# Kernel optimization log

Hardware: AMD Instinct MI355X
Metric: run time of the kernel (lower is better)

Reference implementation:

```python
import jax, jax.numpy as jnp
import numpy as np
import math

EPS = 1e-8      # module eps for log/clamp
BN_EPS = 1e-5   # torch BatchNorm1d default eps


def _bn(h, g, b, m, v):
    # eval-mode BatchNorm1d over channel dim of (B, C, P)
    scale = g / jnp.sqrt(v + BN_EPS)
    return (h - m[None, :, None]) * scale[None, :, None] + b[None, :, None]


def _conv(h, W, b):
    # Conv1d with kernel_size=1 == per-point channel mixing
    return jnp.einsum('oc,bcp->bop', W, h) + b[None, :, None]


def _pairwise_lv_fts(xi, xj, eps=EPS):
    # ParT pairwise Lorentz-vector features, num_outputs=4: (lnkt, lnz, lndelta, lnm2)
    def ptrapphi(p):
        px, py, pz, e = p[:, 0], p[:, 1], p[:, 2], p[:, 3]
        pt = jnp.sqrt(px * px + py * py)
        rap = 0.5 * jnp.log1p(2.0 * pz / jnp.maximum(e - pz, 1e-20))
        phi = jnp.arctan2(py, px)
        return pt, rap, phi

    pti, rapi, phii = ptrapphi(xi)
    ptj, rapj, phij = ptrapphi(xj)
    dphi = jnp.mod(phii - phij + math.pi, 2.0 * math.pi) - math.pi
    delta = jnp.sqrt((rapi - rapj) ** 2 + dphi ** 2)
    lndelta = jnp.log(jnp.maximum(delta, eps))
    ptmin = jnp.minimum(pti, ptj)
    lnkt = jnp.log(jnp.maximum(ptmin * delta, eps))
    lnz = jnp.log(jnp.maximum(ptmin / jnp.maximum(pti + ptj, eps), eps))
    xs = xi + xj
    m2 = jnp.maximum(xs[:, 3] ** 2 - xs[:, 0] ** 2 - xs[:, 1] ** 2 - xs[:, 2] ** 2, eps)
    lnm2 = jnp.log(m2)
    return jnp.stack([lnkt, lnz, lndelta, lnm2], axis=1)  # (B, 4, P)


def setup_inputs():
    key = jax.random.key(0)
    ks = jax.random.split(key, 8)
    B, S = 64, 128
    dims = [64, 64, 64]
    # physically valid 4-vectors: E = sqrt(|p|^2 + m^2), m = 0.1
    p3 = jax.random.normal(ks[0], (B, 3, S), dtype=jnp.float32) * 10.0
    e = jnp.sqrt(jnp.sum(p3 * p3, axis=1, keepdims=True) + 0.01)
    x = jnp.concatenate([p3, e], axis=1)  # (B, 4, S): px, py, pz, E

    def bn_p(k, c):
        k1, k2 = jax.random.split(k)
        return (jnp.ones(c), jnp.zeros(c),
                jax.random.normal(k1, (c,)) * 0.1,
                jax.random.uniform(k2, (c,)) * 0.5 + 0.5)

    inp = {'x': x}
    g, b, m, v = bn_p(ks[1], 4)
    inp.update({'bn0_g': g, 'bn0_b': b, 'bn0_m': m, 'bn0_v': v})
    in_c = 4
    for li, d in enumerate(dims, start=1):
        kw, kb, kbn = jax.random.split(ks[1 + li], 3)
        inp['W%d' % li] = jax.random.normal(kw, (d, in_c)) * (1.0 / np.sqrt(in_c).astype(np.float32))
        inp['b%d' % li] = jax.random.normal(kb, (d,)) * 0.01
        g, b, m, v = bn_p(kbn, d)
        inp['bn%d_g' % li] = g; inp['bn%d_b' % li] = b
        inp['bn%d_m' % li] = m; inp['bn%d_v' % li] = v
        in_c = d
    return inp


def reference(x, bn0_g, bn0_b, bn0_m, bn0_v,
              W1, b1, bn1_g, bn1_b, bn1_m, bn1_v,
              W2, b2, bn2_g, bn2_b, bn2_m, bn2_v,
              W3, b3, bn3_g, bn3_b, bn3_m, bn3_v):
    B, _, S = x.shape
    # symmetric path: lower-triangle pairs incl. diagonal (remove_self_pair=False)
    i, j = np.tril_indices(S, 0)
    xi = x[:, :, i]                      # (B, 4, P) gather
    xj = x[:, :, j]
    fts = _pairwise_lv_fts(xi, xj)       # (B, 4, P)
    h = _bn(fts, bn0_g, bn0_b, bn0_m, bn0_v)
    h = jax.nn.gelu(_bn(_conv(h, W1, b1), bn1_g, bn1_b, bn1_m, bn1_v), approximate=False)
    h = jax.nn.gelu(_bn(_conv(h, W2, b2), bn2_g, bn2_b, bn2_m, bn2_v), approximate=False)
    h = _bn(_conv(h, W3, b3), bn3_g, bn3_b, bn3_m, bn3_v)  # pre-activation output
    out_dim = h.shape[1]
    # scatter back into symmetric (B, out_dim, S, S)
    y = jnp.zeros((B, out_dim, S, S), h.dtype)
    y = y.at[:, :, i, j].set(h)
    y = y.at[:, :, j, i].set(h)
    return y
```

## Files before the change

### kernel.cpp

```cpp
#include <hip/hip_runtime.h>
#include <math.h>

#define S_TOK 128
#define PS_A 72
#define PS_O 257

#define OFF_A1 0
#define OFF_C1 256
#define OFF_C2 320
#define OFF_C3 384
#define OFF_BF 448

using bf16x8 = __attribute__((ext_vector_type(8))) __bf16;
using f32x4  = __attribute__((ext_vector_type(4))) float;

__device__ __forceinline__ unsigned short f2bf(float v) {
    unsigned u = __builtin_bit_cast(unsigned, v);
    u += 0x7fffu + ((u >> 16) & 1u);
    return (unsigned short)(u >> 16);
}

__device__ __forceinline__ float gelu_fast(float v) {
    float v2 = v * v;
    float z  = v * fmaf(0.044715f, v2, 1.0f);
    float u  = z * 2.3022082f;
    float e;
    asm("v_exp_f32 %0, %1" : "=v"(e) : "v"(u));
    float d = e + 1.0f;
    float r;
    asm("v_rcp_f32 %0, %1" : "=v"(r) : "v"(d));
    return fmaf(-v, r, v);
}

__global__ void fold_weights_kernel(
    const float* __restrict__ bn0g, const float* __restrict__ bn0b,
    const float* __restrict__ bn0m, const float* __restrict__ bn0v,
    const float* __restrict__ W1,  const float* __restrict__ b1,
    const float* __restrict__ bn1g, const float* __restrict__ bn1b,
    const float* __restrict__ bn1m, const float* __restrict__ bn1v,
    const float* __restrict__ W2,  const float* __restrict__ b2,
    const float* __restrict__ bn2g, const float* __restrict__ bn2b,
    const float* __restrict__ bn2m, const float* __restrict__ bn2v,
    const float* __restrict__ W3,  const float* __restrict__ b3,
    const float* __restrict__ bn3g, const float* __restrict__ bn3b,
    const float* __restrict__ bn3m, const float* __restrict__ bn3v,
    float* __restrict__ ws)
{
    int o = threadIdx.x;
    if (o >= 64) return;
    float s0[4], t0[4];
    #pragma unroll
    for (int c = 0; c < 4; ++c) {
        float s = bn0g[c] / sqrtf(bn0v[c] + 1e-5f);
        s0[c] = s;
        t0[c] = bn0b[c] - bn0m[c] * s;
    }
    float s1 = bn1g[o] / sqrtf(bn1v[o] + 1e-5f);
    float acc = b1[o] - bn1m[o];
    #pragma unroll
    for (int c = 0; c < 4; ++c) {
        float w = W1[o*4 + c];
        ws[OFF_A1 + o*4 + c] = s1 * w * s0[c];
        acc += w * t0[c];
    }
    ws[OFF_C1 + o] = s1 * acc + bn1b[o];

    unsigned short* wsbf = (unsigned short*)(ws + OFF_BF);
    unsigned short* A2bf = wsbf;
    unsigned short* A3bf = wsbf + 4096;

    float s2 = bn2g[o] / sqrtf(bn2v[o] + 1e-5f);
    for (int c = 0; c < 64; ++c) A2bf[o*64 + c] = f2bf(W2[o*64 + c] * s2);
    ws[OFF_C2 + o] = (b2[o] - bn2m[o]) * s2 + bn2b[o];

    float s3 = bn3g[o] / sqrtf(bn3v[o] + 1e-5f);
    for (int c = 0; c < 64; ++c) A3bf[o*64 + c] = f2bf(W3[o*64 + c] * s3);
    ws[OFF_C3 + o] = (b3[o] - bn3m[o]) * s3 + bn3b[o];
}

__global__ __launch_bounds__(256, 4) void pair_mlp_mfma(
    const float* __restrict__ x, const float* __restrict__ ws,
    float* __restrict__ y)
{
    __shared__ __align__(16) unsigned short Abuf[256 * PS_A];

    const int t = blockIdx.x;
    const int b = blockIdx.y;
    int I = (int)((sqrtf(8.0f * (float)t + 1.0f) - 1.0f) * 0.5f);
    while ((I + 1) * (I + 2) / 2 <= t) ++I;
    while (I * (I + 1) / 2 > t) --I;
    const int J = t - I * (I + 1) / 2;

    const int tid  = threadIdx.x;
    const int lane = tid & 63;
    const int wv   = tid >> 6;
    const int lcol = lane & 15;
    const int lgrp = lane >> 4;

    const int li = tid >> 4;
    const int lj = tid & 15;
    const int i = I * 16 + li;
    const int j = J * 16 + lj;

    const float* xb = x + (size_t)b * 4 * S_TOK;
    const float pxi = xb[0*S_TOK + i], pyi = xb[1*S_TOK + i];
    const float pzi = xb[2*S_TOK + i], ei  = xb[3*S_TOK + i];
    const float pxj = xb[0*S_TOK + j], pyj = xb[1*S_TOK + j];
    const float pzj = xb[2*S_TOK + j], ej  = xb[3*S_TOK + j];

    const float pti = sqrtf(pxi*pxi + pyi*pyi);
    const float ptj = sqrtf(pxj*pxj + pyj*pyj);
    const float rapi = 0.5f * log1pf(2.0f * pzi / fmaxf(ei - pzi, 1e-20f));
    const float rapj = 0.5f * log1pf(2.0f * pzj / fmaxf(ej - pzj, 1e-20f));
    const float phii = atan2f(pyi, pxi);
    const float phij = atan2f(pyj, pxj);

    const float PI_F    = 3.14159265358979323846f;
    const float TWOPI_F = 6.28318530717958647692f;
    float dx   = phii - phij + PI_F;
    float dphi = dx - TWOPI_F * floorf(dx * (1.0f / TWOPI_F)) - PI_F;
    float drap = rapi - rapj;
    float delta = sqrtf(drap*drap + dphi*dphi);
    float lndelta = logf(fmaxf(delta, 1e-8f));
    float ptmin = fminf(pti, ptj);
    float f0 = logf(fmaxf(ptmin * delta, 1e-8f));
    float f1 = logf(fmaxf(ptmin / fmaxf(pti + ptj, 1e-8f), 1e-8f));
    float f2 = lndelta;
    float sx = pxi + pxj, sy = pyi + pyj, sz = pzi + pzj, se = ei + ej;
    float f3 = logf(fmaxf(se*se - sx*sx - sy*sy - sz*sz, 1e-8f));

    const float* A1 = ws + OFF_A1;
    const float* C1 = ws + OFF_C1;
    #pragma unroll
    for (int oc = 0; oc < 8; ++oc) {
        unsigned pk[4];
        #pragma unroll
        for (int q = 0; q < 4; ++q) {
            const int o0 = oc*8 + 2*q;
            float z0 = C1[o0]   + A1[o0*4+0]*f0 + A1[o0*4+1]*f1
                                + A1[o0*4+2]*f2 + A1[o0*4+3]*f3;
            float z1 = C1[o0+1] + A1[(o0+1)*4+0]*f0 + A1[(o0+1)*4+1]*f1
                                + A1[(o0+1)*4+2]*f2 + A1[(o0+1)*4+3]*f3;
            z0 = gelu_fast(z0);
            z1 = gelu_fast(z1);
            pk[q] = (unsigned)f2bf(z0) | ((unsigned)f2bf(z1) << 16);
        }
        uint4 v; v.x = pk[0]; v.y = pk[1]; v.z = pk[2]; v.w = pk[3];
        *reinterpret_cast<uint4*>(&Abuf[tid * PS_A + oc * 8]) = v;
    }
    __syncthreads();

    const unsigned short* A2bf = (const unsigned short*)(ws + OFF_BF);
    const unsigned short* A3bf = A2bf + 4096;
    const float* C2 = ws + OFF_C2;
    const float* C3 = ws + OFF_C3;

    f32x4 acc2[4][4];
    #pragma unroll
    for (int mt = 0; mt < 4; ++mt)
        #pragma unroll
        for (int nt = 0; nt < 4; ++nt)
            acc2[mt][nt] = f32x4{0.f, 0.f, 0.f, 0.f};
    {
        bf16x8 wf[4][2];
        #pragma unroll
        for (int nt = 0; nt < 4; ++nt)
            #pragma unroll
            for (int kt = 0; kt < 2; ++kt)
                wf[nt][kt] = *reinterpret_cast<const bf16x8*>(
                    A2bf + (nt*16 + lcol)*64 + kt*32 + lgrp*8);
        #pragma unroll
        for (int kt = 0; kt < 2; ++kt) {
            bf16x8 af[4];
            #pragma unroll
            for (int mt = 0; mt < 4; ++mt)
                af[mt] = *reinterpret_cast<const bf16x8*>(
                    &Abuf[(wv*64 + mt*16 + lcol)*PS_A + kt*32 + lgrp*8]);
            #pragma unroll
            for (int mt = 0; mt < 4; ++mt)
                #pragma unroll
                for (int nt = 0; nt < 4; ++nt)
                    acc2[mt][nt] = __builtin_amdgcn_mfma_f32_16x16x32_bf16(
                        af[mt], wf[nt][kt], acc2[mt][nt], 0, 0, 0);
        }
    }
    __syncthreads();

    #pragma unroll
    for (int nt = 0; nt < 4; ++nt) {
        const float bias = C2[nt*16 + lcol];
        #pragma unroll
        for (int mt = 0; mt < 4; ++mt)
            #pragma unroll
            for (int r = 0; r < 4; ++r) {
                float z = acc2[mt][nt][r] + bias;
                Abuf[(wv*64 + mt*16 + 4*lgrp + r)*PS_A + nt*16 + lcol]
                    = f2bf(gelu_fast(z));
            }
    }
    __syncthreads();

    f32x4 acc3[4][4];
    #pragma unroll
    for (int mt = 0; mt < 4; ++mt)
        #pragma unroll
        for (int nt = 0; nt < 4; ++nt)
            acc3[mt][nt] = f32x4{0.f, 0.f, 0.f, 0.f};
    {
        bf16x8 wf[4][2];
        #pragma unroll
        for (int nt = 0; nt < 4; ++nt)
            #pragma unroll
            for (int kt = 0; kt < 2; ++kt)
                wf[nt][kt] = *reinterpret_cast<const bf16x8*>(
                    A3bf + (nt*16 + lcol)*64 + kt*32 + lgrp*8);
        #pragma unroll
        for (int kt = 0; kt < 2; ++kt) {
            bf16x8 af[4];
            #pragma unroll
            for (int mt = 0; mt < 4; ++mt)
                af[mt] = *reinterpret_cast<const bf16x8*>(
                    &Abuf[(wv*64 + mt*16 + lcol)*PS_A + kt*32 + lgrp*8]);
            #pragma unroll
            for (int mt = 0; mt < 4; ++mt)
                #pragma unroll
                for (int nt = 0; nt < 4; ++nt)
                    acc3[mt][nt] = __builtin_amdgcn_mfma_f32_16x16x32_bf16(
                        af[mt], wf[nt][kt], acc3[mt][nt], 0, 0, 0);
        }
    }
    __syncthreads();

    float* Obuf = reinterpret_cast<float*>(Abuf);
    const size_t ybase = (size_t)b * 64 * (S_TOK * S_TOK);
    const int jd = tid & 15;
    const int g2 = (tid >> 4) & 3;
    const bool diag = (I == J);

    for (int nt = 0; nt < 4; ++nt) {
        const float bias3 = C3[nt*16 + lcol];
        #pragma unroll
        for (int mt = 0; mt < 4; ++mt) {
            const int il = 4*wv + mt;
            #pragma unroll
            for (int r = 0; r < 4; ++r) {
                const int jl = 4*lgrp + r;
                Obuf[lcol*PS_O + il*16 + ((jl + il) & 15)] = acc3[mt][nt][r] + bias3;
            }
        }
        __syncthreads();
        #pragma unroll
        for (int k = 0; k < 16; ++k) {
            const int ol = 4*(k & 3) + wv;
            const int o  = nt*16 + ol;
            const int il = 4*(k >> 2) + g2;
            const float vdir = Obuf[ol*PS_O + il*16 + ((jd + il) & 15)];
            y[ybase + (size_t)o*(S_TOK*S_TOK) + (16*I + il)*S_TOK + 16*J + jd] = vdir;
        }
        if (!diag) {
            #pragma unroll
            for (int k = 0; k < 16; ++k) {
                const int ol = 4*(k & 3) + wv;
                const int o  = nt*16 + ol;
                const int il = 4*(k >> 2) + g2;
                const float vmir = Obuf[ol*PS_O + jd*16 + ((il + jd) & 15)];
                y[ybase + (size_t)o*(S_TOK*S_TOK) + (16*J + il)*S_TOK + 16*I + jd] = vmir;
            }
        }
        __syncthreads();
    }
}

extern "C" void kernel_launch(void* const* d_in, const int* in_sizes, int n_in,
                              void* d_out, int out_size, void* d_ws, size_t ws_size,
                              hipStream_t stream) {
    const float* x    = (const float*)d_in[0];
    const float* bn0g = (const float*)d_in[1];
    const float* bn0b = (const float*)d_in[2];
    const float* bn0m = (const float*)d_in[3];
    const float* bn0v = (const float*)d_in[4];
    const float* W1   = (const float*)d_in[5];
    const float* b1   = (const float*)d_in[6];
    const float* bn1g = (const float*)d_in[7];
    const float* bn1b = (const float*)d_in[8];
    const float* bn1m = (const float*)d_in[9];
    const float* bn1v = (const float*)d_in[10];
    const float* W2   = (const float*)d_in[11];
    const float* b2   = (const float*)d_in[12];
    const float* bn2g = (const float*)d_in[13];
    const float* bn2b = (const float*)d_in[14];
    const float* bn2m = (const float*)d_in[15];
    const float* bn2v = (const float*)d_in[16];
    const float* W3   = (const float*)d_in[17];
    const float* b3   = (const float*)d_in[18];
    const float* bn3g = (const float*)d_in[19];
    const float* bn3b = (const float*)d_in[20];
    const float* bn3m = (const float*)d_in[21];
    const float* bn3v = (const float*)d_in[22];

    float* ws = (float*)d_ws;
    float* y  = (float*)d_out;

    fold_weights_kernel<<<1, 64, 0, stream>>>(
        bn0g, bn0b, bn0m, bn0v, W1, b1, bn1g, bn1b, bn1m, bn1v,
        W2, b2, bn2g, bn2b, bn2m, bn2v, W3, b3, bn3g, bn3b, bn3m, bn3v, ws);

    dim3 grid(36, 64);
    pair_mlp_mfma<<<grid, 256, 0, stream>>>(x, ws, y);
}
```

Measured before the change: 76.08 us.

## Swizzle LDS activation layout and write direct tile with vector stores

Result: slower. 116.1 us (+52.6%).

```diff
diff --git a/kernel.cpp b/kernel.cpp
--- a/kernel.cpp
+++ b/kernel.cpp
@@ -2,8 +2,9 @@
 #include <math.h>
 
 #define S_TOK 128
-#define PS_A 72
 #define PS_O 257
+
+#define SWZ(row, byteoff) ((((row) * 128) + (byteoff)) ^ (((row) & 7) << 4))
 
 #define OFF_A1 0
 #define OFF_C1 256
@@ -78,11 +79,11 @@
     ws[OFF_C3 + o] = (b3[o] - bn3m[o]) * s3 + bn3b[o];
 }
 
-__global__ __launch_bounds__(256, 4) void pair_mlp_mfma(
+__global__ __launch_bounds__(256, 5) void pair_mlp_mfma(
     const float* __restrict__ x, const float* __restrict__ ws,
     float* __restrict__ y)
 {
-    __shared__ __align__(16) unsigned short Abuf[256 * PS_A];
+    __shared__ __align__(16) unsigned char Abuf[32768];
 
     const int t = blockIdx.x;
     const int b = blockIdx.y;
@@ -146,7 +147,7 @@
             pk[q] = (unsigned)f2bf(z0) | ((unsigned)f2bf(z1) << 16);
         }
         uint4 v; v.x = pk[0]; v.y = pk[1]; v.z = pk[2]; v.w = pk[3];
-        *reinterpret_cast<uint4*>(&Abuf[tid * PS_A + oc * 8]) = v;
+        *reinterpret_cast<uint4*>(Abuf + SWZ(tid, oc*16)) = v;
     }
     __syncthreads();
 
@@ -175,7 +176,7 @@
             #pragma unroll
             for (int mt = 0; mt < 4; ++mt)
                 af[mt] = *reinterpret_cast<const bf16x8*>(
-                    &Abuf[(wv*64 + mt*16 + lcol)*PS_A + kt*32 + lgrp*8]);
+                    Abuf + SWZ(wv*64 + mt*16 + lcol, kt*64 + lgrp*16));
             #pragma unroll
             for (int mt = 0; mt < 4; ++mt)
                 #pragma unroll
@@ -194,7 +195,8 @@
             #pragma unroll
             for (int r = 0; r < 4; ++r) {
                 float z = acc2[mt][nt][r] + bias;
-                Abuf[(wv*64 + mt*16 + 4*lgrp + r)*PS_A + nt*16 + lcol]
+                *reinterpret_cast<unsigned short*>(
+                    Abuf + SWZ(wv*64 + mt*16 + 4*lgrp + r, (nt*16 + lcol)*2))
                     = f2bf(gelu_fast(z));
             }
     }
@@ -220,7 +222,7 @@
             #pragma unroll
             for (int mt = 0; mt < 4; ++mt)
                 af[mt] = *reinterpret_cast<const bf16x8*>(
-                    &Abuf[(wv*64 + mt*16 + lcol)*PS_A + kt*32 + lgrp*8]);
+                    Abuf + SWZ(wv*64 + mt*16 + lcol, kt*64 + lgrp*16));
             #pragma unroll
             for (int mt = 0; mt < 4; ++mt)
                 #pragma unroll
@@ -229,35 +231,44 @@
                         af[mt], wf[nt][kt], acc3[mt][nt], 0, 0, 0);
         }
     }
-    __syncthreads();
-
-    float* Obuf = reinterpret_cast<float*>(Abuf);
+
     const size_t ybase = (size_t)b * 64 * (S_TOK * S_TOK);
-    const int jd = tid & 15;
-    const int g2 = (tid >> 4) & 3;
     const bool diag = (I == J);
 
-    for (int nt = 0; nt < 4; ++nt) {
-        const float bias3 = C3[nt*16 + lcol];
-        #pragma unroll
-        for (int mt = 0; mt < 4; ++mt) {
-            const int il = 4*wv + mt;
-            #pragma unroll
-            for (int r = 0; r < 4; ++r) {
-                const int jl = 4*lgrp + r;
-                Obuf[lcol*PS_O + il*16 + ((jl + il) & 15)] = acc3[mt][nt][r] + bias3;
+    if (diag) {
+        #pragma unroll
+        for (int nt = 0; nt < 4; ++nt) {
+            const float bias3 = C3[nt*16 + lcol];
+            #pragma unroll
+            for (int mt = 0; mt < 4; ++mt) {
+                f32x4 v = acc3[mt][nt] + bias3;
+                *reinterpret_cast<f32x4*>(
+                    &y[ybase + (size_t)(nt*16 + lcol)*(S_TOK*S_TOK)
+                             + (16*I + 4*wv + mt)*S_TOK + 16*J + 4*lgrp]) = v;
             }
         }
+    } else {
+        float* Obuf = reinterpret_cast<float*>(Abuf);
+        const int jd = tid & 15;
+        const int g2 = (tid >> 4) & 3;
         __syncthreads();
-        #pragma unroll
-        for (int k = 0; k < 16; ++k) {
-            const int ol = 4*(k & 3) + wv;
-            const int o  = nt*16 + ol;
-            const int il = 4*(k >> 2) + g2;
-            const float vdir = Obuf[ol*PS_O + il*16 + ((jd + il) & 15)];
-            y[ybase + (size_t)o*(S_TOK*S_TOK) + (16*I + il)*S_TOK + 16*J + jd] = vdir;
-        }
-        if (!diag) {
+
+        for (int nt = 0; nt < 4; ++nt) {
+            const float bias3 = C3[nt*16 + lcol];
+            #pragma unroll
+            for (int mt = 0; mt < 4; ++mt) {
+                f32x4 v = acc3[mt][nt] + bias3;
+                *reinterpret_cast<f32x4*>(
+                    &y[ybase + (size_t)(nt*16 + lcol)*(S_TOK*S_TOK)
+                             + (16*I + 4*wv + mt)*S_TOK + 16*J + 4*lgrp]) = v;
+                const int il = 4*wv + mt;
+                #pragma unroll
+                for (int r = 0; r < 4; ++r) {
+                    const int jl = 4*lgrp + r;
+                    Obuf[lcol*PS_O + il*16 + ((jl + il) & 15)] = v[r];
+                }
+            }
+            __syncthreads();
             #pragma unroll
             for (int k = 0; k < 16; ++k) {
                 const int ol = 4*(k & 3) + wv;
@@ -266,8 +277,8 @@
                 const float vmir = Obuf[ol*PS_O + jd*16 + ((il + jd) & 15)];
                 y[ybase + (size_t)o*(S_TOK*S_TOK) + (16*J + il)*S_TOK + 16*I + jd] = vmir;
             }
-        }
-        __syncthreads();
+            __syncthreads();
+        }
     }
 }
 
```
